# Kernel tuning notes

Measured on AMD Instinct MI355X. Metric: run time of the kernel, lower is better.

## Reference

```python
import jax, jax.numpy as jnp
import numpy as np


def setup_inputs() -> dict:
    key = jax.random.key(0)
    k1, k2 = jax.random.split(key)
    B, Q, T, D = 128, 512, 512, 256
    inputs = jax.random.normal(k1, (B, T, D), dtype=jnp.float32)
    query = jax.random.normal(k2, (B, Q, D), dtype=jnp.float32)
    return {"inputs": inputs, "query": query}


def reference(inputs, query):
    # inputs: [B, T, D] (keys == values), query: [B, Q, D]
    D = inputs.shape[2]
    scale = 1.0 / jnp.sqrt(jnp.asarray(D, dtype=inputs.dtype))
    # scores: [B, Q, T]
    scores = jnp.einsum("bqd,btd->bqt", query, inputs) * scale
    weights = jax.nn.softmax(scores, axis=2)
    # attended: [B, Q, D]
    attended = jnp.einsum("bqt,btd->bqd", weights, inputs)
    # pool over query dim -> [B, D]
    return jnp.sum(attended, axis=1)
```

## Files before the change

### kernel.cpp

```cpp
#include <hip/hip_runtime.h>
#include <hip/hip_bf16.h>


typedef __bf16 bf16x8 __attribute__((ext_vector_type(8)));
typedef float  f32x4  __attribute__((ext_vector_type(4)));
typedef unsigned int u32;

#define B_    128
#define Tn    512
#define Dn    256
#define SCALE 0.0625f

__device__ __forceinline__ int lidx(int row, int ch) {
  return row * 256 + (((ch ^ (row & 31)) & 31) << 3);
}

__device__ __forceinline__ bf16x8 pack8(float4 v0, float4 v1) {
  bf16x8 w;
  w[0] = (__bf16)v0.x; w[1] = (__bf16)v0.y;
  w[2] = (__bf16)v0.z; w[3] = (__bf16)v0.w;
  w[4] = (__bf16)v1.x; w[5] = (__bf16)v1.y;
  w[6] = (__bf16)v1.z; w[7] = (__bf16)v1.w;
  return w;
}

__device__ __forceinline__ void gll16(const __bf16* g, __bf16* l) {
  __builtin_amdgcn_global_load_lds((const u32 __attribute__((address_space(1)))*)g,
                                   (u32 __attribute__((address_space(3)))*)l,
                                   16, 0, 0);
}

__global__ void __launch_bounds__(512) conv_k(const float* __restrict__ inputs,
                                              __bf16* __restrict__ kbf) {
  const int tid = threadIdx.x;
  const int b = blockIdx.x & 127, tile = blockIdx.x >> 7;
#pragma unroll
  for (int i = 0; i < 4; ++i) {
    int c = i * 512 + tid;
    int row = c >> 5, p = c & 31;
    int ch = p ^ (row & 31);
    const float4* s =
        (const float4*)(inputs + ((size_t)b * Tn + tile * 64 + row) * Dn + ch * 8);
    *(bf16x8*)(kbf + (size_t)(b * 8 + tile) * 16384 + (size_t)c * 8) =
        pack8(s[0], s[1]);
  }
}

__global__ void __launch_bounds__(512, 4) attn_qk2(
    const __bf16* __restrict__ kbf, const float* __restrict__ query,
    float* __restrict__ c_ws) {
  __shared__ __bf16 smem[2 * 64 * 256];

  const int tid  = threadIdx.x;
  const int bidx = blockIdx.x;
  const int b  = bidx & 127;
  const int qt = bidx >> 7;

  const int wave = tid >> 6, lane = tid & 63;
  const int quad = lane >> 4, l15 = lane & 15;
  const int qg = wave >> 1;
  const int th = wave & 1;

  __bf16* Kb0 = smem;
  __bf16* Kb1 = smem + 64 * 256;

  const __bf16* kbase = kbf + (size_t)b * (8 * 16384) + (wave * 64 + lane) * 8;

#pragma unroll
  for (int i = 0; i < 4; ++i)
    gll16(kbase + i * 4096, Kb0 + i * 4096 + wave * 512);

  const float* qsrc = query + ((size_t)b * 512 + qt * 64 + qg * 16 + l15) * Dn;
  bf16x8 a_[8];
#pragma unroll
  for (int dc = 0; dc < 8; ++dc) {
    const float4* p = (const float4*)(qsrc + dc * 32 + quad * 8);
    a_[dc] = pack8(p[0], p[1]);
  }

  f32x4 acc[16];
  f32x4 zero = {0.f, 0.f, 0.f, 0.f};
#pragma unroll
  for (int i = 0; i < 16; ++i) acc[i] = zero;

  __syncthreads();

#pragma unroll
  for (int tt = 0; tt < 8; ++tt) {
    if (tt < 7) {
      const __bf16* gs = kbase + (tt + 1) * 16384;
      __bf16* ld = (tt & 1) ? Kb0 : Kb1;
#pragma unroll
      for (int i = 0; i < 4; ++i)
        gll16(gs + i * 4096, ld + i * 4096 + wave * 512);
    }
    const __bf16* cur = (tt & 1) ? Kb1 : Kb0;
#pragma unroll
    for (int dc = 0; dc < 8; ++dc) {
#pragma unroll
      for (int ct = 0; ct < 2; ++ct) {
        bf16x8 bb =
            *(const bf16x8*)(cur + lidx(th * 32 + ct * 16 + l15, dc * 4 + quad));
        acc[tt * 2 + ct] = __builtin_amdgcn_mfma_f32_16x16x32_bf16(
            a_[dc], bb, acc[tt * 2 + ct], 0, 0, 0);
      }
    }
    __syncthreads();
  }

  float* lred  = (float*)smem;
  float* cpart = (float*)smem + 128;

  float rs[4] = {0.f, 0.f, 0.f, 0.f};
#pragma unroll
  for (int ti = 0; ti < 16; ++ti)
#pragma unroll
    for (int r = 0; r < 4; ++r) {
      float p = __expf(acc[ti][r] * SCALE);
      acc[ti][r] = p;
      rs[r] += p;
    }
#pragma unroll
  for (int off = 1; off <= 8; off <<= 1)
#pragma unroll
    for (int r = 0; r < 4; ++r) rs[r] += __shfl_xor(rs[r], off);

  if (l15 == 0) {
#pragma unroll
    for (int r = 0; r < 4; ++r)
      lred[(qg * 2 + th) * 16 + quad * 4 + r] = rs[r];
  }
  __syncthreads();

  float linv[4];
#pragma unroll
  for (int r = 0; r < 4; ++r) {
    int row = quad * 4 + r;
    linv[r] =
        1.f / (lred[(qg * 2 + 0) * 16 + row] + lred[(qg * 2 + 1) * 16 + row]);
  }

#pragma unroll
  for (int tt = 0; tt < 8; ++tt)
#pragma unroll
    for (int ct = 0; ct < 2; ++ct) {
      float v = 0.f;
#pragma unroll
      for (int r = 0; r < 4; ++r) v += acc[tt * 2 + ct][r] * linv[r];
      v += __shfl_xor(v, 16);
      v += __shfl_xor(v, 32);
      if (quad == 0)
        cpart[qg * 512 + tt * 64 + th * 32 + ct * 16 + l15] = v;
    }
  __syncthreads();

  float* cout = c_ws + ((size_t)qt * B_ + b) * Tn;
  cout[tid] = cpart[tid] + cpart[512 + tid] + cpart[1024 + tid] + cpart[1536 + tid];
}

template <int NSL>
__global__ void __launch_bounds__(256) attn_av(
    const float* __restrict__ inputs, const float* __restrict__ c_ws,
    float* __restrict__ out) {
  __shared__ float cs[64];
  __shared__ float psum[3][256];
  const int bid = blockIdx.x, tid = threadIdx.x;
  const int b = bid & 127, sl = bid >> 7;

  if (tid < 64) {
    int t = sl * 64 + tid;
    float s = 0.f;
#pragma unroll
    for (int i = 0; i < NSL; ++i) s += c_ws[(size_t)(i * B_ + b) * Tn + t];
    cs[tid] = s;
  }
  __syncthreads();

  const int w = tid >> 6, d4 = tid & 63;
  const float4* vb =
      (const float4*)(inputs + ((size_t)b * Tn + sl * 64 + w * 16) * Dn) + d4;
  float ox = 0.f, oy = 0.f, oz = 0.f, ow = 0.f;
#pragma unroll
  for (int j = 0; j < 16; ++j) {
    float c = cs[w * 16 + j];
    float4 v = vb[(size_t)j * 64];
    ox += c * v.x; oy += c * v.y; oz += c * v.z; ow += c * v.w;
  }
  if (w) {
    float4 t = {ox, oy, oz, ow};
    *(float4*)&psum[w - 1][d4 * 4] = t;
  }
  __syncthreads();
  if (!w) {
    float4 p0 = *(float4*)&psum[0][d4 * 4];
    float4 p1 = *(float4*)&psum[1][d4 * 4];
    float4 p2 = *(float4*)&psum[2][d4 * 4];
    float* op = out + b * 256 + d4 * 4;
    atomicAdd(op + 0, ox + p0.x + p1.x + p2.x);
    atomicAdd(op + 1, oy + p0.y + p1.y + p2.y);
    atomicAdd(op + 2, oz + p0.z + p1.z + p2.z);
    atomicAdd(op + 3, ow + p0.w + p1.w + p2.w);
  }
}

__device__ __forceinline__ void kload(const float* __restrict__ src, int tid,
                                      float4* pre) {
#pragma unroll
  for (int i = 0; i < 4; ++i) {
    int u = i * 512 + tid;
    int row = u >> 5, ch = u & 31;
    const float4* p = (const float4*)(src + row * 256 + ch * 8);
    pre[2 * i]     = p[0];
    pre[2 * i + 1] = p[1];
  }
}

__device__ __forceinline__ void kstore(__bf16* dst, int tid,
                                       const float4* pre) {
#pragma unroll
  for (int i = 0; i < 4; ++i) {
    int u = i * 512 + tid;
    int row = u >> 5, ch = u & 31;
    *(bf16x8*)(dst + lidx(row, ch)) = pack8(pre[2 * i], pre[2 * i + 1]);
  }
}

__global__ void __launch_bounds__(512, 2) attn_qk(
    const float* __restrict__ inputs, const float* __restrict__ query,
    float* __restrict__ c_ws) {
  __shared__ __bf16 smem[128 * 256 + 2 * 64 * 256];
  __bf16* Qs = smem;
  __bf16* Kb[2] = {smem + 128 * 256, smem + 128 * 256 + 64 * 256};

  const int tid  = threadIdx.x;
  const int bidx = blockIdx.x;
  const int b  = bidx & 127;
  const int qt = bidx >> 7;

  const float* qsrc = query  + ((size_t)b * 512 + (size_t)qt * 128) * Dn;
  const float* ksrc = inputs + (size_t)b * Tn * Dn;

  const int wave = tid >> 6, lane = tid & 63;
  const int quad = lane >> 4, l15 = lane & 15;
  const int qg = wave >> 1;
  const int th = wave & 1;

  float4 pre[2][8];
  kload(ksrc, tid, pre[0]);

#pragma unroll
  for (int i = 0; i < 8; ++i) {
    int u = i * 512 + tid;
    int row = u >> 5, ch = u & 31;
    const float4* p = (const float4*)(qsrc + row * 256 + ch * 8);
    *(bf16x8*)(Qs + lidx(row, ch)) = pack8(p[0], p[1]);
  }

  kload(ksrc + (size_t)1 * 64 * Dn, tid, pre[1]);
  __syncthreads();

  kstore(Kb[0], tid, pre[0]);
  kload(ksrc + (size_t)2 * 64 * Dn, tid, pre[0]);
  __syncthreads();

  f32x4 acc[8][2][2];
  f32x4 zero = {0.f, 0.f, 0.f, 0.f};
#pragma unroll
  for (int tt = 0; tt < 8; ++tt)
#pragma unroll
    for (int ct = 0; ct < 2; ++ct) {
      acc[tt][ct][0] = zero;
      acc[tt][ct][1] = zero;
    }

#pragma unroll
  for (int tt = 0; tt < 8; ++tt) {
    if (tt < 7) kstore(Kb[(tt + 1) & 1], tid, pre[(tt + 1) & 1]);
    if (tt < 5) kload(ksrc + (size_t)(tt + 3) * 64 * Dn, tid, pre[(tt + 1) & 1]);

    const __bf16* cur = Kb[tt & 1];
#pragma unroll
    for (int dc = 0; dc < 8; ++dc) {
      bf16x8 a0 = *(const bf16x8*)(Qs + lidx(qg * 32 + l15, dc * 4 + quad));
      bf16x8 a1 = *(const bf16x8*)(Qs + lidx(qg * 32 + 16 + l15, dc * 4 + quad));
#pragma unroll
      for (int ct = 0; ct < 2; ++ct) {
        bf16x8 bb =
            *(const bf16x8*)(cur + lidx(th * 32 + ct * 16 + l15, dc * 4 + quad));
        acc[tt][ct][0] = __builtin_amdgcn_mfma_f32_16x16x32_bf16(
            a0, bb, acc[tt][ct][0], 0, 0, 0);
        acc[tt][ct][1] = __builtin_amdgcn_mfma_f32_16x16x32_bf16(
            a1, bb, acc[tt][ct][1], 0, 0, 0);
      }
    }
    __syncthreads();
  }

  float* lred  = (float*)Kb[0];
  float* cpart = (float*)Kb[0] + 256;

  float rs[2][4];
#pragma unroll
  for (int m = 0; m < 2; ++m)
#pragma unroll
    for (int r = 0; r < 4; ++r) rs[m][r] = 0.f;
#pragma unroll
  for (int tt = 0; tt < 8; ++tt)
#pragma unroll
    for (int ct = 0; ct < 2; ++ct)
#pragma unroll
      for (int m = 0; m < 2; ++m)
#pragma unroll
        for (int r = 0; r < 4; ++r) {
          float p = __expf(acc[tt][ct][m][r] * SCALE);
          acc[tt][ct][m][r] = p;
          rs[m][r] += p;
        }
#pragma unroll
  for (int off = 1; off <= 8; off <<= 1)
#pragma unroll
    for (int m = 0; m < 2; ++m)
#pragma unroll
      for (int r = 0; r < 4; ++r) rs[m][r] += __shfl_xor(rs[m][r], off);

  if (l15 == 0) {
#pragma unroll
    for (int m = 0; m < 2; ++m)
#pragma unroll
      for (int r = 0; r < 4; ++r)
        lred[(qg * 2 + th) * 32 + m * 16 + quad * 4 + r] = rs[m][r];
  }
  __syncthreads();

  float linv[2][4];
#pragma unroll
  for (int m = 0; m < 2; ++m)
#pragma unroll
    for (int r = 0; r < 4; ++r) {
      int row = m * 16 + quad * 4 + r;
      linv[m][r] =
          1.f / (lred[(qg * 2 + 0) * 32 + row] + lred[(qg * 2 + 1) * 32 + row]);
    }

#pragma unroll
  for (int tt = 0; tt < 8; ++tt)
#pragma unroll
    for (int ct = 0; ct < 2; ++ct) {
      float v = 0.f;
#pragma unroll
      for (int m = 0; m < 2; ++m)
#pragma unroll
        for (int r = 0; r < 4; ++r) v += acc[tt][ct][m][r] * linv[m][r];
      v += __shfl_xor(v, 16);
      v += __shfl_xor(v, 32);
      if (quad == 0)
        cpart[qg * 512 + tt * 64 + th * 32 + ct * 16 + l15] = v;
    }
  __syncthreads();

  float* cout = c_ws + ((size_t)qt * B_ + b) * Tn;
#pragma unroll
  for (int t = tid; t < 512; t += 256) {
    if (t < 512)
      cout[t] = cpart[t] + cpart[512 + t] + cpart[1024 + t] + cpart[1536 + t];
  }
}

extern "C" void kernel_launch(void* const* d_in, const int* in_sizes, int n_in,
                              void* d_out, int out_size, void* d_ws, size_t ws_size,
                              hipStream_t stream) {
  const float* inputs = (const float*)d_in[0];
  const float* query  = (const float*)d_in[1];
  float* out  = (float*)d_out;

  hipMemsetAsync(out, 0, (size_t)B_ * Dn * sizeof(float), stream);

  const size_t cbytes8 = (size_t)8 * B_ * Tn * sizeof(float);
  const size_t kbytes  = (size_t)B_ * Tn * Dn * sizeof(__bf16);
  if (ws_size >= cbytes8 + kbytes) {
    float*  c_ws = (float*)d_ws;
    __bf16* kbf  = (__bf16*)((char*)d_ws + cbytes8);
    conv_k <<<dim3(1024), dim3(512), 0, stream>>>(inputs, kbf);
    attn_qk2<<<dim3(1024), dim3(512), 0, stream>>>(kbf, query, c_ws);
    attn_av<8><<<dim3(1024), dim3(256), 0, stream>>>(inputs, c_ws, out);
  } else {
    float* c_ws = (float*)d_ws;
    attn_qk<<<dim3(512), dim3(512), 0, stream>>>(inputs, query, c_ws);
    attn_av<4><<<dim3(1024), dim3(256), 0, stream>>>(inputs, c_ws, out);
  }
}
```

Baseline: 194.2 us.

## Fuse score and value passes into one kernel with 4-stage LDS pipeline

```diff
diff --git a/kernel.cpp b/kernel.cpp
--- a/kernel.cpp
+++ b/kernel.cpp
@@ -10,6 +10,11 @@
 #define Tn    512
 #define Dn    256
 #define SCALE 0.0625f
+
+#define WAITV4 asm volatile("s_waitcnt vmcnt(4)" ::: "memory")
+#define WAITV2 asm volatile("s_waitcnt vmcnt(2)" ::: "memory")
+#define WAITV0 asm volatile("s_waitcnt vmcnt(0)" ::: "memory")
+#define BARRAW __builtin_amdgcn_s_barrier()
 
 __device__ __forceinline__ int lidx(int row, int ch) {
   return row * 256 + (((ch ^ (row & 31)) & 31) << 3);
@@ -46,10 +51,14 @@
   }
 }
 
-__global__ void __launch_bounds__(512, 4) attn_qk2(
+__global__ void __launch_bounds__(512, 4) attn_fused(
     const __bf16* __restrict__ kbf, const float* __restrict__ query,
-    float* __restrict__ c_ws) {
-  __shared__ __bf16 smem[2 * 64 * 256];
+    float* __restrict__ out) {
+  __shared__ __bf16 smem[4 * 8192 + 2688 * 2];
+  float* scratch = (float*)(smem + 4 * 8192);
+  float* lred  = scratch;
+  float* cpart = scratch + 128;
+  float* cfin  = scratch + 2176;
 
   const int tid  = threadIdx.x;
   const int bidx = blockIdx.x;
@@ -61,14 +70,18 @@
   const int qg = wave >> 1;
   const int th = wave & 1;
 
-  __bf16* Kb0 = smem;
-  __bf16* Kb1 = smem + 64 * 256;
-
-  const __bf16* kbase = kbf + (size_t)b * (8 * 16384) + (wave * 64 + lane) * 8;
-
-#pragma unroll
-  for (int i = 0; i < 4; ++i)
-    gll16(kbase + i * 4096, Kb0 + i * 4096 + wave * 512);
+  const __bf16* ksrc = kbf + (size_t)b * 131072;
+
+#define STAGE(t)                                                        \
+  {                                                                     \
+    _Pragma("unroll") for (int i_ = 0; i_ < 2; ++i_) {                  \
+      int s_ = wave * 2 + i_;                                           \
+      gll16(ksrc + (size_t)(t) * 8192 + s_ * 512 + lane * 8,            \
+            smem + ((t) & 3) * 8192 + s_ * 512);                        \
+    }                                                                   \
+  }
+
+  STAGE(0);
 
   const float* qsrc = query + ((size_t)b * 512 + qt * 64 + qg * 16 + l15) * Dn;
   bf16x8 a_[8];
@@ -78,38 +91,31 @@
     a_[dc] = pack8(p[0], p[1]);
   }
 
+  STAGE(1);
+  STAGE(2);
+
   f32x4 acc[16];
   f32x4 zero = {0.f, 0.f, 0.f, 0.f};
 #pragma unroll
   for (int i = 0; i < 16; ++i) acc[i] = zero;
 
-  __syncthreads();
-
-#pragma unroll
-  for (int tt = 0; tt < 8; ++tt) {
-    if (tt < 7) {
-      const __bf16* gs = kbase + (tt + 1) * 16384;
-      __bf16* ld = (tt & 1) ? Kb0 : Kb1;
-#pragma unroll
-      for (int i = 0; i < 4; ++i)
-        gll16(gs + i * 4096, ld + i * 4096 + wave * 512);
-    }
-    const __bf16* cur = (tt & 1) ? Kb1 : Kb0;
+#pragma unroll
+  for (int tt = 0; tt < 16; ++tt) {
+    if (tt <= 13) { WAITV4; } else if (tt == 14) { WAITV2; } else { WAITV0; }
+    BARRAW;
+    if (tt < 13) STAGE(tt + 3);
+    const __bf16* cur = smem + (tt & 3) * 8192;
 #pragma unroll
     for (int dc = 0; dc < 8; ++dc) {
-#pragma unroll
-      for (int ct = 0; ct < 2; ++ct) {
-        bf16x8 bb =
-            *(const bf16x8*)(cur + lidx(th * 32 + ct * 16 + l15, dc * 4 + quad));
-        acc[tt * 2 + ct] = __builtin_amdgcn_mfma_f32_16x16x32_bf16(
-            a_[dc], bb, acc[tt * 2 + ct], 0, 0, 0);
-      }
-    }
-    __syncthreads();
-  }
-
-  float* lred  = (float*)smem;
-  float* cpart = (float*)smem + 128;
+      bf16x8 bb = *(const bf16x8*)(cur + lidx(th * 16 + l15, dc * 4 + quad));
+      acc[tt] = __builtin_amdgcn_mfma_f32_16x16x32_bf16(a_[dc], bb, acc[tt],
+                                                        0, 0, 0);
+    }
+  }
+
+  STAGE(0);
+  STAGE(1);
+  STAGE(2);
 
   float rs[4] = {0.f, 0.f, 0.f, 0.f};
 #pragma unroll
@@ -141,12 +147,207 @@
   }
 
 #pragma unroll
+  for (int ti = 0; ti < 16; ++ti) {
+    float v = 0.f;
+#pragma unroll
+    for (int r = 0; r < 4; ++r) v += acc[ti][r] * linv[r];
+    v += __shfl_xor(v, 16);
+    v += __shfl_xor(v, 32);
+    if (quad == 0) cpart[qg * 512 + ti * 32 + th * 16 + l15] = v;
+  }
+  __syncthreads();
+
+  cfin[tid] = cpart[tid] + cpart[512 + tid] + cpart[1024 + tid] +
+              cpart[1536 + tid];
+  __syncthreads();
+
+  const int dchunk = tid & 31;
+  const int tgrp   = tid >> 5;
+  float o[8] = {0.f, 0.f, 0.f, 0.f, 0.f, 0.f, 0.f, 0.f};
+
+#pragma unroll
+  for (int tt = 0; tt < 16; ++tt) {
+    if (tt <= 13) { WAITV4; } else if (tt == 14) { WAITV2; } else { WAITV0; }
+    BARRAW;
+    if (tt < 13) STAGE(tt + 3);
+    const __bf16* cur = smem + (tt & 3) * 8192;
+#pragma unroll
+    for (int rr = 0; rr < 2; ++rr) {
+      int row = tgrp * 2 + rr;
+      float c = cfin[tt * 32 + row];
+      bf16x8 v = *(const bf16x8*)(cur + lidx(row, dchunk));
+#pragma unroll
+      for (int j = 0; j < 8; ++j) o[j] += c * (float)v[j];
+    }
+  }
+  __syncthreads();
+
+  float* ored = (float*)smem;
+  f32x4 o0 = {o[0], o[1], o[2], o[3]}, o1 = {o[4], o[5], o[6], o[7]};
+  *(f32x4*)&ored[tgrp * 260 + dchunk * 8]     = o0;
+  *(f32x4*)&ored[tgrp * 260 + dchunk * 8 + 4] = o1;
+  __syncthreads();
+  if (tid < 256) {
+    float s = 0.f;
+#pragma unroll
+    for (int g = 0; g < 16; ++g) s += ored[g * 260 + tid];
+    atomicAdd(out + (size_t)b * 256 + tid, s);
+  }
+#undef STAGE
+}
+
+__device__ __forceinline__ int lidx64(int row, int ch) {
+  return row * 256 + (((ch ^ (row & 31)) & 31) << 3);
+}
+
+__device__ __forceinline__ void kload(const float* __restrict__ src, int tid,
+                                      float4* pre) {
+#pragma unroll
+  for (int i = 0; i < 4; ++i) {
+    int u = i * 512 + tid;
+    int row = u >> 5, ch = u & 31;
+    const float4* p = (const float4*)(src + row * 256 + ch * 8);
+    pre[2 * i]     = p[0];
+    pre[2 * i + 1] = p[1];
+  }
+}
+
+__device__ __forceinline__ void kstore(__bf16* dst, int tid,
+                                       const float4* pre) {
+#pragma unroll
+  for (int i = 0; i < 4; ++i) {
+    int u = i * 512 + tid;
+    int row = u >> 5, ch = u & 31;
+    *(bf16x8*)(dst + lidx64(row, ch)) = pack8(pre[2 * i], pre[2 * i + 1]);
+  }
+}
+
+__global__ void __launch_bounds__(512, 2) attn_qk(
+    const float* __restrict__ inputs, const float* __restrict__ query,
+    float* __restrict__ c_ws) {
+  __shared__ __bf16 smem[128 * 256 + 2 * 64 * 256];
+  __bf16* Qs = smem;
+  __bf16* Kb[2] = {smem + 128 * 256, smem + 128 * 256 + 64 * 256};
+
+  const int tid  = threadIdx.x;
+  const int bidx = blockIdx.x;
+  const int b  = bidx & 127;
+  const int qt = bidx >> 7;
+
+  const float* qsrc = query  + ((size_t)b * 512 + (size_t)qt * 128) * Dn;
+  const float* ksrc = inputs + (size_t)b * Tn * Dn;
+
+  const int wave = tid >> 6, lane = tid & 63;
+  const int quad = lane >> 4, l15 = lane & 15;
+  const int qg = wave >> 1;
+  const int th = wave & 1;
+
+  float4 pre[2][8];
+  kload(ksrc, tid, pre[0]);
+
+#pragma unroll
+  for (int i = 0; i < 8; ++i) {
+    int u = i * 512 + tid;
+    int row = u >> 5, ch = u & 31;
+    const float4* p = (const float4*)(qsrc + row * 256 + ch * 8);
+    *(bf16x8*)(Qs + lidx64(row, ch)) = pack8(p[0], p[1]);
+  }
+
+  kload(ksrc + (size_t)1 * 64 * Dn, tid, pre[1]);
+  __syncthreads();
+
+  kstore(Kb[0], tid, pre[0]);
+  kload(ksrc + (size_t)2 * 64 * Dn, tid, pre[0]);
+  __syncthreads();
+
+  f32x4 acc[8][2][2];
+  f32x4 zero = {0.f, 0.f, 0.f, 0.f};
+#pragma unroll
+  for (int tt = 0; tt < 8; ++tt)
+#pragma unroll
+    for (int ct = 0; ct < 2; ++ct) {
+      acc[tt][ct][0] = zero;
+      acc[tt][ct][1] = zero;
+    }
+
+#pragma unroll
+  for (int tt = 0; tt < 8; ++tt) {
+    if (tt < 7) kstore(Kb[(tt + 1) & 1], tid, pre[(tt + 1) & 1]);
+    if (tt < 5) kload(ksrc + (size_t)(tt + 3) * 64 * Dn, tid, pre[(tt + 1) & 1]);
+
+    const __bf16* cur = Kb[tt & 1];
+#pragma unroll
+    for (int dc = 0; dc < 8; ++dc) {
+      bf16x8 a0 = *(const bf16x8*)(Qs + lidx64(qg * 32 + l15, dc * 4 + quad));
+      bf16x8 a1 = *(const bf16x8*)(Qs + lidx64(qg * 32 + 16 + l15, dc * 4 + quad));
+#pragma unroll
+      for (int ct = 0; ct < 2; ++ct) {
+        bf16x8 bb =
+            *(const bf16x8*)(cur + lidx64(th * 32 + ct * 16 + l15, dc * 4 + quad));
+        acc[tt][ct][0] = __builtin_amdgcn_mfma_f32_16x16x32_bf16(
+            a0, bb, acc[tt][ct][0], 0, 0, 0);
+        acc[tt][ct][1] = __builtin_amdgcn_mfma_f32_16x16x32_bf16(
+            a1, bb, acc[tt][ct][1], 0, 0, 0);
+      }
+    }
+    __syncthreads();
+  }
+
+  float* lred  = (float*)Kb[0];
+  float* cpart = (float*)Kb[0] + 256;
+
+  float rs[2][4];
+#pragma unroll
+  for (int m = 0; m < 2; ++m)
+#pragma unroll
+    for (int r = 0; r < 4; ++r) rs[m][r] = 0.f;
+#pragma unroll
+  for (int tt = 0; tt < 8; ++tt)
+#pragma unroll
+    for (int ct = 0; ct < 2; ++ct)
+#pragma unroll
+      for (int m = 0; m < 2; ++m)
+#pragma unroll
+        for (int r = 0; r < 4; ++r) {
+          float p = __expf(acc[tt][ct][m][r] * SCALE);
+          acc[tt][ct][m][r] = p;
+          rs[m][r] += p;
+        }
+#pragma unroll
+  for (int off = 1; off <= 8; off <<= 1)
+#pragma unroll
+    for (int m = 0; m < 2; ++m)
+#pragma unroll
+      for (int r = 0; r < 4; ++r) rs[m][r] += __shfl_xor(rs[m][r], off);
+
+  if (l15 == 0) {
+#pragma unroll
+    for (int m = 0; m < 2; ++m)
+#pragma unroll
+      for (int r = 0; r < 4; ++r)
+        lred[(qg * 2 + th) * 32 + m * 16 + quad * 4 + r] = rs[m][r];
+  }
+  __syncthreads();
+
+  float linv[2][4];
+#pragma unroll
+  for (int m = 0; m < 2; ++m)
+#pragma unroll
+    for (int r = 0; r < 4; ++r) {
+      int row = m * 16 + quad * 4 + r;
+      linv[m][r] =
+          1.f / (lred[(qg * 2 + 0) * 32 + row] + lred[(qg * 2 + 1) * 32 + row]);
+    }
+
+#pragma unroll
   for (int tt = 0; tt < 8; ++tt)
 #pragma unroll
     for (int ct = 0; ct < 2; ++ct) {
       float v = 0.f;
 #pragma unroll
-      for (int r = 0; r < 4; ++r) v += acc[tt * 2 + ct][r] * linv[r];
+      for (int m = 0; m < 2; ++m)
+#pragma unroll
+        for (int r = 0; r < 4; ++r) v += acc[tt][ct][m][r] * linv[m][r];
       v += __shfl_xor(v, 16);
       v += __shfl_xor(v, 32);
       if (quad == 0)
@@ -155,7 +356,11 @@
   __syncthreads();
 
   float* cout = c_ws + ((size_t)qt * B_ + b) * Tn;
-  cout[tid] = cpart[tid] + cpart[512 + tid] + cpart[1024 + tid] + cpart[1536 + tid];
+#pragma unroll
+  for (int t = tid; t < 512; t += 256) {
+    if (t < 512)
+      cout[t] = cpart[t] + cpart[512 + t] + cpart[1024 + t] + cpart[1536 + t];
+  }
 }
 
 template <int NSL>
@@ -203,169 +408,6 @@
   }
 }
 
-__device__ __forceinline__ void kload(const float* __restrict__ src, int tid,
-                                      float4* pre) {
-#pragma unroll
-  for (int i = 0; i < 4; ++i) {
-    int u = i * 512 + tid;
-    int row = u >> 5, ch = u & 31;
-    const float4* p = (const float4*)(src + row * 256 + ch * 8);
-    pre[2 * i]     = p[0];
-    pre[2 * i + 1] = p[1];
-  }
-}
-
-__device__ __forceinline__ void kstore(__bf16* dst, int tid,
-                                       const float4* pre) {
-#pragma unroll
-  for (int i = 0; i < 4; ++i) {
-    int u = i * 512 + tid;
-    int row = u >> 5, ch = u & 31;
-    *(bf16x8*)(dst + lidx(row, ch)) = pack8(pre[2 * i], pre[2 * i + 1]);
-  }
-}
-
-__global__ void __launch_bounds__(512, 2) attn_qk(
-    const float* __restrict__ inputs, const float* __restrict__ query,
-    float* __restrict__ c_ws) {
-  __shared__ __bf16 smem[128 * 256 + 2 * 64 * 256];
-  __bf16* Qs = smem;
-  __bf16* Kb[2] = {smem + 128 * 256, smem + 128 * 256 + 64 * 256};
-
-  const int tid  = threadIdx.x;
-  const int bidx = blockIdx.x;
-  const int b  = bidx & 127;
-  const int qt = bidx >> 7;
-
-  const float* qsrc = query  + ((size_t)b * 512 + (size_t)qt * 128) * Dn;
-  const float* ksrc = inputs + (size_t)b * Tn * Dn;
-
-  const int wave = tid >> 6, lane = tid & 63;
-  const int quad = lane >> 4, l15 = lane & 15;
-  const int qg = wave >> 1;
-  const int th = wave & 1;
-
-  float4 pre[2][8];
-  kload(ksrc, tid, pre[0]);
-
-#pragma unroll
-  for (int i = 0; i < 8; ++i) {
-    int u = i * 512 + tid;
-    int row = u >> 5, ch = u & 31;
-    const float4* p = (const float4*)(qsrc + row * 256 + ch * 8);
-    *(bf16x8*)(Qs + lidx(row, ch)) = pack8(p[0], p[1]);
-  }
-
-  kload(ksrc + (size_t)1 * 64 * Dn, tid, pre[1]);
-  __syncthreads();
-
-  kstore(Kb[0], tid, pre[0]);
-  kload(ksrc + (size_t)2 * 64 * Dn, tid, pre[0]);
-  __syncthreads();
-
-  f32x4 acc[8][2][2];
-  f32x4 zero = {0.f, 0.f, 0.f, 0.f};
-#pragma unroll
-  for (int tt = 0; tt < 8; ++tt)
-#pragma unroll
-    for (int ct = 0; ct < 2; ++ct) {
-      acc[tt][ct][0] = zero;
-      acc[tt][ct][1] = zero;
-    }
-
-#pragma unroll
-  for (int tt = 0; tt < 8; ++tt) {
-    if (tt < 7) kstore(Kb[(tt + 1) & 1], tid, pre[(tt + 1) & 1]);
-    if (tt < 5) kload(ksrc + (size_t)(tt + 3) * 64 * Dn, tid, pre[(tt + 1) & 1]);
-
-    const __bf16* cur = Kb[tt & 1];
-#pragma unroll
-    for (int dc = 0; dc < 8; ++dc) {
-      bf16x8 a0 = *(const bf16x8*)(Qs + lidx(qg * 32 + l15, dc * 4 + quad));
-      bf16x8 a1 = *(const bf16x8*)(Qs + lidx(qg * 32 + 16 + l15, dc * 4 + quad));
-#pragma unroll
-      for (int ct = 0; ct < 2; ++ct) {
-        bf16x8 bb =
-            *(const bf16x8*)(cur + lidx(th * 32 + ct * 16 + l15, dc * 4 + quad));
-        acc[tt][ct][0] = __builtin_amdgcn_mfma_f32_16x16x32_bf16(
-            a0, bb, acc[tt][ct][0], 0, 0, 0);
-        acc[tt][ct][1] = __builtin_amdgcn_mfma_f32_16x16x32_bf16(
-            a1, bb, acc[tt][ct][1], 0, 0, 0);
-      }
-    }
-    __syncthreads();
-  }
-
-  float* lred  = (float*)Kb[0];
-  float* cpart = (float*)Kb[0] + 256;
-
-  float rs[2][4];
-#pragma unroll
-  for (int m = 0; m < 2; ++m)
-#pragma unroll
-    for (int r = 0; r < 4; ++r) rs[m][r] = 0.f;
-#pragma unroll
-  for (int tt = 0; tt < 8; ++tt)
-#pragma unroll
-    for (int ct = 0; ct < 2; ++ct)
-#pragma unroll
-      for (int m = 0; m < 2; ++m)
-#pragma unroll
-        for (int r = 0; r < 4; ++r) {
-          float p = __expf(acc[tt][ct][m][r] * SCALE);
-          acc[tt][ct][m][r] = p;
-          rs[m][r] += p;
-        }
-#pragma unroll
-  for (int off = 1; off <= 8; off <<= 1)
-#pragma unroll
-    for (int m = 0; m < 2; ++m)
-#pragma unroll
-      for (int r = 0; r < 4; ++r) rs[m][r] += __shfl_xor(rs[m][r], off);
-
-  if (l15 == 0) {
-#pragma unroll
-    for (int m = 0; m < 2; ++m)
-#pragma unroll
-      for (int r = 0; r < 4; ++r)
-        lred[(qg * 2 + th) * 32 + m * 16 + quad * 4 + r] = rs[m][r];
-  }
-  __syncthreads();
-
-  float linv[2][4];
-#pragma unroll
-  for (int m = 0; m < 2; ++m)
-#pragma unroll
-    for (int r = 0; r < 4; ++r) {
-      int row = m * 16 + quad * 4 + r;
-      linv[m][r] =
-          1.f / (lred[(qg * 2 + 0) * 32 + row] + lred[(qg * 2 + 1) * 32 + row]);
-    }
-
-#pragma unroll
-  for (int tt = 0; tt < 8; ++tt)
-#pragma unroll
-    for (int ct = 0; ct < 2; ++ct) {
-      float v = 0.f;
-#pragma unroll
-      for (int m = 0; m < 2; ++m)
-#pragma unroll
-        for (int r = 0; r < 4; ++r) v += acc[tt][ct][m][r] * linv[m][r];
-      v += __shfl_xor(v, 16);
-      v += __shfl_xor(v, 32);
-      if (quad == 0)
-        cpart[qg * 512 + tt * 64 + th * 32 + ct * 16 + l15] = v;
-    }
-  __syncthreads();
-
-  float* cout = c_ws + ((size_t)qt * B_ + b) * Tn;
-#pragma unroll
-  for (int t = tid; t < 512; t += 256) {
-    if (t < 512)
-      cout[t] = cpart[t] + cpart[512 + t] + cpart[1024 + t] + cpart[1536 + t];
-  }
-}
-
 extern "C" void kernel_launch(void* const* d_in, const int* in_sizes, int n_in,
                               void* d_out, int out_size, void* d_ws, size_t ws_size,
                               hipStream_t stream) {
@@ -375,14 +417,11 @@
 
   hipMemsetAsync(out, 0, (size_t)B_ * Dn * sizeof(float), stream);
 
-  const size_t cbytes8 = (size_t)8 * B_ * Tn * sizeof(float);
-  const size_t kbytes  = (size_t)B_ * Tn * Dn * sizeof(__bf16);
-  if (ws_size >= cbytes8 + kbytes) {
-    float*  c_ws = (float*)d_ws;
-    __bf16* kbf  = (__bf16*)((char*)d_ws + cbytes8);
-    conv_k <<<dim3(1024), dim3(512), 0, stream>>>(inputs, kbf);
-    attn_qk2<<<dim3(1024), dim3(512), 0, stream>>>(kbf, query, c_ws);
-    attn_av<8><<<dim3(1024), dim3(256), 0, stream>>>(inputs, c_ws, out);
+  const size_t kbytes = (size_t)B_ * Tn * Dn * sizeof(__bf16);
+  if (ws_size >= kbytes) {
+    __bf16* kbf = (__bf16*)d_ws;
+    conv_k    <<<dim3(1024), dim3(512), 0, stream>>>(inputs, kbf);
+    attn_fused<<<dim3(1024), dim3(512), 0, stream>>>(kbf, query, out);
   } else {
     float* c_ws = (float*)d_ws;
     attn_qk<<<dim3(512), dim3(512), 0, stream>>>(inputs, query, c_ws);
```

After: 246.0 us. +26.7%, slower.
